# Optimization experiments

Measured on AMD Instinct MI355X. Metric: run time of the kernel, lower is better.

## Reference

```python
import jax, jax.numpy as jnp
import numpy as np

KS = 4          # kernel_size per pseudo-dim (open linear B-splines, degree 1)
GRID = 28       # level-0 grid side
BATCH = 256     # number of graphs
NUM_FIRST_FC = 49


def _grid(n, B):
    """Batched 8-neighborhood grid graph with 2D pseudo-coords in [0,1]."""
    rs, cs = np.meshgrid(np.arange(n), np.arange(n), indexing='ij')
    idx = rs * n + cs
    src_l, dst_l, ps_l = [], [], []
    for dr in (-1, 0, 1):
        for dc in (-1, 0, 1):
            if dr == 0 and dc == 0:
                continue
            r2, c2 = rs + dr, cs + dc
            ok = (r2 >= 0) & (r2 < n) & (c2 >= 0) & (c2 < n)
            src_l.append(idx[ok])
            dst_l.append((r2 * n + c2)[ok])
            m = int(ok.sum())
            ps_l.append(np.stack([np.full(m, (dr + 1) / 2.0),
                                  np.full(m, (dc + 1) / 2.0)], 1))
    src = np.concatenate(src_l)
    dst = np.concatenate(dst_l)
    pseudo = np.concatenate(ps_l).astype(np.float32)
    off = (np.arange(B) * n * n)[:, None]
    src_b = (src[None] + off).reshape(-1)
    dst_b = (dst[None] + off).reshape(-1)
    return (np.stack([src_b, dst_b]).astype(np.int32),
            np.tile(pseudo, (B, 1)))


def _cluster(n, B):
    """Factor-4 (2x2 block) graclus-style cluster assignment, batched."""
    rs, cs = np.meshgrid(np.arange(n), np.arange(n), indexing='ij')
    c = ((rs // 2) * (n // 2) + (cs // 2)).reshape(-1)
    off = (np.arange(B) * (n // 2) ** 2)[:, None]
    return (c[None] + off).reshape(-1).astype(np.int32)


def setup_inputs() -> dict:
    key = jax.random.key(0)
    ks = jax.random.split(key, 16)
    e0, p0 = _grid(GRID, BATCH)          # 28x28 level
    e1, p1 = _grid(GRID // 2, BATCH)     # 14x14 level
    c0 = _cluster(GRID, BATCH)           # 784 -> 196 per graph
    c1 = _cluster(GRID // 2, BATCH)      # 196 -> 49 per graph
    N0 = BATCH * GRID * GRID
    s = 0.1
    inp = {
        'x': jax.random.normal(ks[0], (N0, 1), jnp.float32),
        'edge_index0': jnp.asarray(e0), 'pseudo0': jnp.asarray(p0),
        'edge_index1': jnp.asarray(e1), 'pseudo1': jnp.asarray(p1),
        'cluster0': jnp.asarray(c0), 'cluster1': jnp.asarray(c1),
        'W1': s * jax.random.normal(ks[1], (16, 1, 32), jnp.float32),
        'root1': s * jax.random.normal(ks[2], (1, 32), jnp.float32),
        'b1': jnp.zeros((32,), jnp.float32),
        'W2': s * jax.random.normal(ks[3], (16, 32, 32), jnp.float32),
        'root2': s * jax.random.normal(ks[4], (32, 32), jnp.float32),
        'b2': jnp.zeros((32,), jnp.float32),
        'W3': s * jax.random.normal(ks[5], (16, 32, 64), jnp.float32),
        'root3': s * jax.random.normal(ks[6], (32, 64), jnp.float32),
        'b3': jnp.zeros((64,), jnp.float32),
        'W4': s * jax.random.normal(ks[7], (16, 64, 64), jnp.float32),
        'root4': s * jax.random.normal(ks[8], (64, 64), jnp.float32),
        'b4': jnp.zeros((64,), jnp.float32),
        'fc1_W': s * jax.random.normal(ks[9], (NUM_FIRST_FC * 64, 512), jnp.float32),
        'fc1_b': jnp.zeros((512,), jnp.float32),
        'fc2_W': s * jax.random.normal(ks[10], (512, 10), jnp.float32),
        'fc2_b': jnp.zeros((10,), jnp.float32),
    }
    return inp


def spline_conv(x, src, dst, pseudo, W, root, bias):
    """SplineGCN layer: degree-1 open B-spline weighting over 2D pseudo-coords,
    mean aggregation over incoming edges, plus root weight and bias."""
    n = x.shape[0]
    pos = pseudo * (KS - 1)                       # [E,2] in [0, KS-1]
    i0f = jnp.clip(jnp.floor(pos), 0, KS - 2)
    frac = pos - i0f                              # [E,2]
    i0 = i0f.astype(jnp.int32)
    XW = jnp.einsum('ni,kio->kno', x, W)          # [K, N, out]: per-kernel transform
    msg = jnp.zeros((src.shape[0], W.shape[2]), x.dtype)
    for a in (0, 1):
        wa = frac[:, 0] if a else 1.0 - frac[:, 0]
        for b in (0, 1):
            wb = frac[:, 1] if b else 1.0 - frac[:, 1]
            k = (i0[:, 0] + a) * KS + (i0[:, 1] + b)     # flat kernel index [E]
            msg = msg + (wa * wb)[:, None] * XW[k, src]  # gather per-edge
    agg = jax.ops.segment_sum(msg, dst, num_segments=n)
    deg = jax.ops.segment_sum(jnp.ones_like(dst, dtype=x.dtype), dst,
                              num_segments=n)
    return agg / jnp.maximum(deg, 1.0)[:, None] + x @ root + bias


def pool4(x, cluster):
    # GraclusMaxPool(2): two halving levels == factor-4 cluster max-pool
    return jax.ops.segment_max(x, cluster, num_segments=x.shape[0] // 4)


def reference(x, edge_index0, pseudo0, edge_index1, pseudo1, cluster0, cluster1,
              W1, root1, b1, W2, root2, b2, W3, root3, b3, W4, root4, b4,
              fc1_W, fc1_b, fc2_W, fc2_b):
    s0, d0 = edge_index0[0], edge_index0[1]
    s1, d1 = edge_index1[0], edge_index1[1]
    h = jax.nn.elu(spline_conv(x, s0, d0, pseudo0, W1, root1, b1))
    h = jax.nn.elu(spline_conv(h, s0, d0, pseudo0, W2, root2, b2))
    h = pool4(h, cluster0)
    h = jax.nn.elu(spline_conv(h, s1, d1, pseudo1, W3, root3, b3))
    h = jax.nn.elu(spline_conv(h, s1, d1, pseudo1, W4, root4, b4))
    h = pool4(h, cluster1)
    h = h.reshape(-1, NUM_FIRST_FC * 64)           # [B, 49*64]
    h = jax.nn.elu(h @ fc1_W + fc1_b)
    # dropout is identity in eval / deterministic reference
    logits = h @ fc2_W + fc2_b
    return jax.nn.log_softmax(logits, axis=-1)
```

## Files before the change

### kernel.cpp

```cpp
#include <hip/hip_runtime.h>

typedef unsigned short u16;
typedef short bf16x8 __attribute__((ext_vector_type(8)));
typedef float f32x4 __attribute__((ext_vector_type(4)));

__device__ __constant__ const int DRS[8] = {-1,-1,-1, 0, 0, 1, 1, 1};
__device__ __constant__ const int DCS[8] = {-1, 0, 1,-1, 1,-1, 0, 1};

__device__ inline float bf2f(u16 u) { return __uint_as_float(((unsigned)u) << 16); }
__device__ inline u16 f2bf(float f) {
  unsigned u = __float_as_uint(f);
  return (u16)((u + 0x7fffu + ((u >> 16) & 1u)) >> 16);
}
__device__ inline float eluf(float v) { return v > 0.f ? v : (__expf(v) - 1.f); }
__device__ inline unsigned pk2(float a, float b) {
  return (unsigned)f2bf(a) | ((unsigned)f2bf(b) << 16);
}

__device__ inline float weff_val(const float* __restrict__ W, int d, int off, int stride) {
  int dd = d >= 4 ? d + 1 : d;
  int dr = dd / 3 - 1, dc = dd - (dd / 3) * 3 - 1;
  int kr0, kr1, nr; float wr0, wr1;
  if (dr < 0)       { kr0 = 0; wr0 = 1.f; kr1 = 0; wr1 = 0.f; nr = 1; }
  else if (dr == 0) { kr0 = 1; wr0 = .5f; kr1 = 2; wr1 = .5f; nr = 2; }
  else              { kr0 = 3; wr0 = 1.f; kr1 = 0; wr1 = 0.f; nr = 1; }
  int kc0, kc1, nc; float wc0, wc1;
  if (dc < 0)       { kc0 = 0; wc0 = 1.f; kc1 = 0; wc1 = 0.f; nc = 1; }
  else if (dc == 0) { kc0 = 1; wc0 = .5f; kc1 = 2; wc1 = .5f; nc = 2; }
  else              { kc0 = 3; wc0 = 1.f; kc1 = 0; wc1 = 0.f; nc = 1; }
  float acc = wr0 * wc0 * W[(kr0 * 4 + kc0) * stride + off];
  if (nc == 2) acc += wr0 * wc1 * W[(kr0 * 4 + kc1) * stride + off];
  if (nr == 2) {
    acc += wr1 * wc0 * W[(kr1 * 4 + kc0) * stride + off];
    if (nc == 2) acc += wr1 * wc1 * W[(kr1 * 4 + kc1) * stride + off];
  }
  return acc;
}

__device__ inline int kperm32(int p) { return (p >> 1) + ((p & 1) << 4); }

__global__ __launch_bounds__(256) void pack_all(
    const float* __restrict__ W1,
    const float* __restrict__ W2, const float* __restrict__ rt2,
    const float* __restrict__ W3, const float* __restrict__ rt3,
    const float* __restrict__ W4, const float* __restrict__ rt4,
    const float* __restrict__ fcW,
    float* __restrict__ wf1, u16* __restrict__ wp2,
    u16* __restrict__ wp3, u16* __restrict__ wp4, u16* __restrict__ wfc) {
  __shared__ u16 T[32 * 514];
  int blk = blockIdx.x, t = threadIdx.x;
  if (blk < 98) {
    int q = blk;
#pragma unroll
    for (int i = 0; i < 16; ++i) {
      int idx = i * 1024 + t * 4;
      int k = idx >> 9, n = idx & 511;
      float4 v = *reinterpret_cast<const float4*>(fcW + (size_t)(q * 32 + k) * 512 + n);
      T[k * 514 + n]     = f2bf(v.x);
      T[k * 514 + n + 1] = f2bf(v.y);
      T[k * 514 + n + 2] = f2bf(v.z);
      T[k * 514 + n + 3] = f2bf(v.w);
    }
    __syncthreads();
#pragma unroll
    for (int w = 0; w < 8; ++w) {
      int g = w * 256 + t;
      int nt = g >> 6, l = g & 63;
      union { int4 q4; u16 s[8]; } R;
#pragma unroll
      for (int j = 0; j < 8; ++j)
        R.s[j] = T[((l >> 4) * 8 + j) * 514 + nt * 16 + (l & 15)];
      *reinterpret_cast<int4*>(wfc + ((size_t)(q * 32 + nt) * 64 + l) * 8) = R.q4;
    }
    return;
  }
  int idx = (blk - 98) * 256 + t;
  if (idx < 256) {
    int d = idx >> 5, o = idx & 31;
    wf1[idx] = weff_val(W1, d, o, 32);
    return;
  }
  if (idx < 9472) {
    int local = idx - 256;
    int j = local & 7, l = (local >> 3) & 63, chunk = local >> 9;
    int ct = chunk & 1, tap = chunk >> 1;
    int k = (l >> 4) * 8 + j, n = ct * 16 + (l & 15);
    float v = tap < 8 ? weff_val(W2, tap, k * 32 + n, 1024) : rt2[k * 32 + n];
    wp2[local] = f2bf(v);
    return;
  }
  if (idx < 27904) {
    int local = idx - 9472;
    int j = local & 7, l = (local >> 3) & 63, chunk = local >> 9;
    int ct = chunk & 3, tap = chunk >> 2;
    int k = kperm32((l >> 4) * 8 + j), n = ct * 16 + (l & 15);
    float v = tap < 8 ? weff_val(W3, tap, k * 64 + n, 2048) : rt3[k * 64 + n];
    wp3[local] = f2bf(v);
    return;
  }
  if (idx < 64768) {
    int local = idx - 27904;
    int j = local & 7, l = (local >> 3) & 63, chunk = local >> 9;
    int q = chunk & 1, tmp = chunk >> 1;
    int ct = tmp & 3, tap = tmp >> 2;
    int k = q * 32 + kperm32((l >> 4) * 8 + j), n = ct * 16 + (l & 15);
    float v = tap < 8 ? weff_val(W4, tap, k * 64 + n, 4096) : rt4[k * 64 + n];
    wp4[local] = f2bf(v);
  }
}

__global__ __launch_bounds__(1024, 2) void conv_mega(
    const float* __restrict__ x,
    const float* __restrict__ wf1, const float* __restrict__ rt1, const float* __restrict__ b1,
    const u16* __restrict__ wp2, const float* __restrict__ b2,
    const u16* __restrict__ wp3, const float* __restrict__ b3,
    const u16* __restrict__ wp4, const float* __restrict__ b4,
    u16* __restrict__ A6) {
  extern __shared__ char smem[];
  int4* H1 = (int4*)smem;
  int4* H3 = (int4*)smem;
  u16*  H5 = (u16*)(smem + 17408);
  int4* H4 = (int4*)(smem + 42496);
  unsigned* H4u = (unsigned*)(smem + 42496);
  float* XT = (float*)(smem + 61568);
  int4*     H2 = (int4*)(smem + 75520);
  unsigned* H2u = (unsigned*)(smem + 75520);

  int img = blockIdx.x, tid = threadIdx.x;
  int lane = tid & 63, wid = tid >> 6;
  int kcb = lane >> 4, n0 = lane & 15;
  int4 z4 = make_int4(0, 0, 0, 0);
  f32x4 zz = {0.f, 0.f, 0.f, 0.f};

  for (int i = tid; i < 3848; i += 1024) H1[i] = z4;
  if (tid < 960) {
    int r = tid >> 5, c = tid & 31;
    bool in = (r >= 1) && (r <= 28) && (c >= 1) && (c <= 28);
    XT[tid] = in ? x[(size_t)img * 784 + (r - 1) * 28 + (c - 1)] : 0.f;
  }
  __syncthreads();

  if (tid < 784) {
    int px = tid;
    int r = px / 28, c = px - 28 * (px / 28);
    float acc[32];
#pragma unroll
    for (int o = 0; o < 32; ++o) acc[o] = 0.f;
#pragma unroll
    for (int d = 0; d < 8; ++d) {
      float xv = XT[(r + 1 - DRS[d]) * 32 + (c + 1 - DCS[d])];
#pragma unroll
      for (int o = 0; o < 32; ++o) acc[o] = fmaf(xv, wf1[d * 32 + o], acc[o]);
    }
    float inv = 1.f / (float)((3 - (r == 0) - (r == 27)) * (3 - (c == 0) - (c == 27)) - 1);
    float xc = XT[(r + 1) * 32 + c + 1];
    unsigned pk[16];
#pragma unroll
    for (int h = 0; h < 16; ++h)
      pk[h] = pk2(eluf(acc[2 * h] * inv + xc * rt1[2 * h] + b1[2 * h]),
                  eluf(acc[2 * h + 1] * inv + xc * rt1[2 * h + 1] + b1[2 * h + 1]));
#pragma unroll
    for (int kc = 0; kc < 4; ++kc)
      H1[kc * 962 + (r + 1) * 32 + (c + 1)] =
          make_int4(pk[4 * kc], pk[4 * kc + 1], pk[4 * kc + 2], pk[4 * kc + 3]);
  }
  __syncthreads();

  {
    bf16x8 w2[9][2];
#pragma unroll
    for (int tap = 0; tap < 9; ++tap)
#pragma unroll
      for (int ct = 0; ct < 2; ++ct)
        w2[tap][ct] = *(const bf16x8*)(wp2 + (tap * 2 + ct) * 512 + lane * 8);
    for (int t = wid; t < 49; t += 16) {
      int pxm = t * 16 + n0;
      int r = pxm / 28, c = pxm - 28 * (pxm / 28);
      f32x4 an[2] = {zz, zz}, ar[2] = {zz, zz};
#pragma unroll
      for (int d = 0; d < 8; ++d) {
        bf16x8 a = *(const bf16x8*)&H1[kcb * 962 + (r + 1 - DRS[d]) * 32 + (c + 1 - DCS[d])];
        an[0] = __builtin_amdgcn_mfma_f32_16x16x32_bf16(a, w2[d][0], an[0], 0, 0, 0);
        an[1] = __builtin_amdgcn_mfma_f32_16x16x32_bf16(a, w2[d][1], an[1], 0, 0, 0);
      }
      {
        bf16x8 a = *(const bf16x8*)&H1[kcb * 962 + (r + 1) * 32 + (c + 1)];
        ar[0] = __builtin_amdgcn_mfma_f32_16x16x32_bf16(a, w2[8][0], ar[0], 0, 0, 0);
        ar[1] = __builtin_amdgcn_mfma_f32_16x16x32_bf16(a, w2[8][1], ar[1], 0, 0, 0);
      }
#pragma unroll
      for (int j = 0; j < 4; ++j) {
        int pm = t * 16 + (lane >> 4) * 4 + j;
        int rm = pm / 28, cm = pm - 28 * (pm / 28);
        float inv = 1.f / (float)((3 - (rm == 0) - (rm == 27)) * (3 - (cm == 0) - (cm == 27)) - 1);
        H2u[pm * 16 + n0] = pk2(eluf(an[0][j] * inv + ar[0][j] + b2[n0]),
                                eluf(an[1][j] * inv + ar[1][j] + b2[16 + n0]));
      }
    }
  }
  __syncthreads();

  for (int i = tid; i < 1032; i += 1024) {
    int kc = i & 3, rem = i >> 2;
    int4 v = z4;
    if (rem < 256) {
      int pr = rem >> 4, pc = rem & 15;
      if (pr >= 1 && pr <= 14 && pc >= 1 && pc <= 14) {
        int px0 = (2 * (pr - 1)) * 28 + 2 * (pc - 1);
        union { int4 q; u16 s[8]; } A, B, C, D, R;
        A.q = H2[px0 * 4 + kc]; B.q = H2[(px0 + 1) * 4 + kc];
        C.q = H2[(px0 + 28) * 4 + kc]; D.q = H2[(px0 + 29) * 4 + kc];
#pragma unroll
        for (int e = 0; e < 8; ++e)
          R.s[e] = f2bf(fmaxf(fmaxf(bf2f(A.s[e]), bf2f(B.s[e])),
                              fmaxf(bf2f(C.s[e]), bf2f(D.s[e]))));
        v = R.q;
      }
    }
    H3[kc * 258 + rem] = v;
  }
  for (int i = tid; i < 2064; i += 1024) H4[i] = z4;
  __syncthreads();

  {
    int ct0 = wid & 1, t0 = wid >> 1;
    bf16x8 w3[9][2];
#pragma unroll
    for (int tap = 0; tap < 9; ++tap)
#pragma unroll
      for (int cc = 0; cc < 2; ++cc)
        w3[tap][cc] = *(const bf16x8*)(wp3 + (tap * 4 + ct0 * 2 + cc) * 512 + lane * 8);
    for (int t = t0; t < 13; t += 8) {
      int pxm = t * 16 + n0; if (pxm > 195) pxm = 195;
      int r = pxm / 14, c = pxm - 14 * (pxm / 14);
      f32x4 an[2] = {zz, zz}, ar[2] = {zz, zz};
#pragma unroll
      for (int d = 0; d < 8; ++d) {
        bf16x8 a = *(const bf16x8*)&H3[kcb * 258 + (r + 1 - DRS[d]) * 16 + (c + 1 - DCS[d])];
        an[0] = __builtin_amdgcn_mfma_f32_16x16x32_bf16(a, w3[d][0], an[0], 0, 0, 0);
        an[1] = __builtin_amdgcn_mfma_f32_16x16x32_bf16(a, w3[d][1], an[1], 0, 0, 0);
      }
      {
        bf16x8 a = *(const bf16x8*)&H3[kcb * 258 + (r + 1) * 16 + (c + 1)];
        ar[0] = __builtin_amdgcn_mfma_f32_16x16x32_bf16(a, w3[8][0], ar[0], 0, 0, 0);
        ar[1] = __builtin_amdgcn_mfma_f32_16x16x32_bf16(a, w3[8][1], ar[1], 0, 0, 0);
      }
#pragma unroll
      for (int j = 0; j < 4; ++j) {
        int pm = t * 16 + (lane >> 4) * 4 + j;
        if (pm < 196) {
          int rm = pm / 14, cm = pm - 14 * (pm / 14);
          float inv = 1.f / (float)((3 - (rm == 0) - (rm == 13)) * (3 - (cm == 0) - (cm == 13)) - 1);
          unsigned v = pk2(eluf(an[0][j] * inv + ar[0][j] + b3[ct0 * 32 + n0]),
                           eluf(an[1][j] * inv + ar[1][j] + b3[ct0 * 32 + 16 + n0]));
          H4u[((ct0 * 4 + (n0 >> 2)) * 258 + (rm + 1) * 16 + (cm + 1)) * 4 + (n0 & 3)] = v;
        }
      }
    }
  }
  __syncthreads();

  {
    int ctg = wid & 3, t0 = wid >> 2;
    bf16x8 w4[9][2];
#pragma unroll
    for (int tap = 0; tap < 9; ++tap)
#pragma unroll
      for (int kq = 0; kq < 2; ++kq)
        w4[tap][kq] = *(const bf16x8*)(wp4 + ((tap * 4 + ctg) * 2 + kq) * 512 + lane * 8);
    for (int t = t0; t < 13; t += 4) {
      int pxm = t * 16 + n0; if (pxm > 195) pxm = 195;
      int r = pxm / 14, c = pxm - 14 * (pxm / 14);
      f32x4 an = zz, ar = zz;
#pragma unroll
      for (int d = 0; d < 8; ++d) {
        int rr = r + 1 - DRS[d], c2 = c + 1 - DCS[d];
#pragma unroll
        for (int kq = 0; kq < 2; ++kq) {
          bf16x8 a = *(const bf16x8*)&H4[(kq * 4 + kcb) * 258 + rr * 16 + c2];
          an = __builtin_amdgcn_mfma_f32_16x16x32_bf16(a, w4[d][kq], an, 0, 0, 0);
        }
      }
#pragma unroll
      for (int kq = 0; kq < 2; ++kq) {
        bf16x8 a = *(const bf16x8*)&H4[(kq * 4 + kcb) * 258 + (r + 1) * 16 + (c + 1)];
        ar = __builtin_amdgcn_mfma_f32_16x16x32_bf16(a, w4[8][kq], ar, 0, 0, 0);
      }
#pragma unroll
      for (int j = 0; j < 4; ++j) {
        int pm = t * 16 + (lane >> 4) * 4 + j;
        if (pm < 196) {
          int rm = pm / 14, cm = pm - 14 * (pm / 14);
          float inv = 1.f / (float)((3 - (rm == 0) - (rm == 13)) * (3 - (cm == 0) - (cm == 13)) - 1);
          int n = ctg * 16 + n0;
          H5[pm * 64 + n] = f2bf(eluf(an[j] * inv + ar[j] + b4[n]));
        }
      }
    }
  }
  __syncthreads();

  if (tid < 392) {
    int kc = tid & 7, q = tid >> 3;
    int r2 = q / 7, c2 = q - 7 * (q / 7);
    int px0 = (2 * r2) * 14 + 2 * c2;
    union { int4 q4; u16 s[8]; } A, B, C, D, R;
    A.q4 = *(const int4*)&H5[px0 * 64 + kc * 8];
    B.q4 = *(const int4*)&H5[(px0 + 1) * 64 + kc * 8];
    C.q4 = *(const int4*)&H5[(px0 + 14) * 64 + kc * 8];
    D.q4 = *(const int4*)&H5[(px0 + 15) * 64 + kc * 8];
#pragma unroll
    for (int e = 0; e < 8; ++e)
      R.s[e] = f2bf(fmaxf(fmaxf(bf2f(A.s[e]), bf2f(B.s[e])),
                          fmaxf(bf2f(C.s[e]), bf2f(D.s[e]))));
    *(int4*)(A6 + ((size_t)img * 49 + q) * 64 + kc * 8) = R.q4;
  }
}

__global__ __launch_bounds__(128) void fc1_mfma(
    const u16* __restrict__ A6, const u16* __restrict__ wfc,
    const float* __restrict__ fc1b, u16* __restrict__ h) {
  int blk = blockIdx.x;
  int mt = blk & 15, bn = blk >> 4;
  int lane = threadIdx.x & 63, w = threadIdx.x >> 6;
  int NT = bn * 2 + w;
  f32x4 acc0 = {0.f, 0.f, 0.f, 0.f}, acc1 = {0.f, 0.f, 0.f, 0.f};
  const u16* Ab = A6 + (size_t)(mt * 16 + (lane & 15)) * 3136 + (lane >> 4) * 8;
  const u16* Bb = wfc + (size_t)NT * 512 + (size_t)lane * 8;
#pragma unroll 7
  for (int qq = 0; qq < 98; qq += 2) {
    bf16x8 a0 = *(const bf16x8*)(Ab + qq * 32);
    bf16x8 b0 = *(const bf16x8*)(Bb + (size_t)qq * 16384);
    acc0 = __builtin_amdgcn_mfma_f32_16x16x32_bf16(a0, b0, acc0, 0, 0, 0);
    bf16x8 a1 = *(const bf16x8*)(Ab + qq * 32 + 32);
    bf16x8 b1 = *(const bf16x8*)(Bb + (size_t)qq * 16384 + 16384);
    acc1 = __builtin_amdgcn_mfma_f32_16x16x32_bf16(a1, b1, acc1, 0, 0, 0);
  }
#pragma unroll
  for (int j = 0; j < 4; ++j) {
    int row = mt * 16 + (lane >> 4) * 4 + j;
    int col = NT * 16 + (lane & 15);
    float v = acc0[j] + acc1[j] + fc1b[col];
    h[(size_t)row * 512 + col] = f2bf(eluf(v));
  }
}

__global__ __launch_bounds__(64) void fc2_kernel(
    const u16* __restrict__ h, const float* __restrict__ W,
    const float* __restrict__ bias, float* __restrict__ out) {
  int bb = blockIdx.x;
  int t = threadIdx.x;
  float acc[10];
#pragma unroll
  for (int o = 0; o < 10; ++o) acc[o] = 0.f;
  bf16x8 hv = *(const bf16x8*)(h + (size_t)bb * 512 + t * 8);
#pragma unroll
  for (int kk = 0; kk < 8; ++kk) {
    float xv = bf2f((u16)hv[kk]);
    int k = t * 8 + kk;
#pragma unroll
    for (int o = 0; o < 10; ++o) acc[o] = fmaf(xv, W[k * 10 + o], acc[o]);
  }
#pragma unroll
  for (int o = 0; o < 10; ++o) {
    float v = acc[o];
#pragma unroll
    for (int s = 32; s >= 1; s >>= 1) v += __shfl_xor(v, s);
    acc[o] = v + bias[o];
  }
  float m = acc[0];
#pragma unroll
  for (int o = 1; o < 10; ++o) m = fmaxf(m, acc[o]);
  float sum = 0.f;
#pragma unroll
  for (int o = 0; o < 10; ++o) sum += __expf(acc[o] - m);
  float lse = m + __logf(sum);
  if (t < 10) out[bb * 10 + t] = acc[t] - lse;
}

extern "C" void kernel_launch(void* const* d_in, const int* in_sizes, int n_in,
                              void* d_out, int out_size, void* d_ws, size_t ws_size,
                              hipStream_t stream) {
  const float* x    = (const float*)d_in[0];
  const float* W1   = (const float*)d_in[7];
  const float* r1   = (const float*)d_in[8];
  const float* b1   = (const float*)d_in[9];
  const float* W2   = (const float*)d_in[10];
  const float* r2   = (const float*)d_in[11];
  const float* b2   = (const float*)d_in[12];
  const float* W3   = (const float*)d_in[13];
  const float* r3   = (const float*)d_in[14];
  const float* b3   = (const float*)d_in[15];
  const float* W4   = (const float*)d_in[16];
  const float* r4   = (const float*)d_in[17];
  const float* b4   = (const float*)d_in[18];
  const float* fc1W = (const float*)d_in[19];
  const float* fc1b = (const float*)d_in[20];
  const float* fc2W = (const float*)d_in[21];
  const float* fc2b = (const float*)d_in[22];

  char* wsb = (char*)d_ws;
  float* wf1  = (float*)(wsb + 0);
  u16*   wp2  = (u16*)(wsb + 1024);
  u16*   wp3  = (u16*)(wsb + 19456);
  u16*   wp4  = (u16*)(wsb + 56320);
  u16*   wfc  = (u16*)(wsb + 130048);
  u16*   A6   = (u16*)(wsb + 3341312);
  u16*   hbuf = (u16*)(wsb + 4946944);

  pack_all<<<351, 256, 0, stream>>>(W1, W2, r2, W3, r3, W4, r4, fc1W,
                                    wf1, wp2, wp3, wp4, wfc);

  (void)hipFuncSetAttribute((const void*)conv_mega,
                            hipFuncAttributeMaxDynamicSharedMemorySize, 125696);
  conv_mega<<<256, 1024, 125696, stream>>>(x, wf1, r1, b1, wp2, b2, wp3, b3,
                                           wp4, b4, A6);

  fc1_mfma<<<256, 128, 0, stream>>>(A6, wfc, fc1b, hbuf);
  fc2_kernel<<<256, 64, 0, stream>>>(hbuf, fc2W, fc2b, (float*)d_out);
}
```

Measured before the change: 53.14 us.

## Move fc1 weight packing into conv kernel and restructure conv4 weight loads

The fc1 weight transpose and bf16 conversion moves out of the pack kernel into the first 98 blocks of the conv megakernel, with smem reused before the conv phases begin. The pack kernel shrinks to the small conv weights, so the conv kernel can start sooner. Conv4 now assigns two column tiles per wave and streams the B fragments from global memory instead of preloading 18 register fragments, cutting register pressure. The costs are extra preamble work in some conv blocks, which causes load imbalance, and repeated global or cache weight loads inside the MFMA loop.

```diff
diff --git a/kernel.cpp b/kernel.cpp
--- a/kernel.cpp
+++ b/kernel.cpp
@@ -39,42 +39,14 @@
 
 __device__ inline int kperm32(int p) { return (p >> 1) + ((p & 1) << 4); }
 
-__global__ __launch_bounds__(256) void pack_all(
+__global__ __launch_bounds__(256) void pack_small(
     const float* __restrict__ W1,
     const float* __restrict__ W2, const float* __restrict__ rt2,
     const float* __restrict__ W3, const float* __restrict__ rt3,
     const float* __restrict__ W4, const float* __restrict__ rt4,
-    const float* __restrict__ fcW,
     float* __restrict__ wf1, u16* __restrict__ wp2,
-    u16* __restrict__ wp3, u16* __restrict__ wp4, u16* __restrict__ wfc) {
-  __shared__ u16 T[32 * 514];
-  int blk = blockIdx.x, t = threadIdx.x;
-  if (blk < 98) {
-    int q = blk;
-#pragma unroll
-    for (int i = 0; i < 16; ++i) {
-      int idx = i * 1024 + t * 4;
-      int k = idx >> 9, n = idx & 511;
-      float4 v = *reinterpret_cast<const float4*>(fcW + (size_t)(q * 32 + k) * 512 + n);
-      T[k * 514 + n]     = f2bf(v.x);
-      T[k * 514 + n + 1] = f2bf(v.y);
-      T[k * 514 + n + 2] = f2bf(v.z);
-      T[k * 514 + n + 3] = f2bf(v.w);
-    }
-    __syncthreads();
-#pragma unroll
-    for (int w = 0; w < 8; ++w) {
-      int g = w * 256 + t;
-      int nt = g >> 6, l = g & 63;
-      union { int4 q4; u16 s[8]; } R;
-#pragma unroll
-      for (int j = 0; j < 8; ++j)
-        R.s[j] = T[((l >> 4) * 8 + j) * 514 + nt * 16 + (l & 15)];
-      *reinterpret_cast<int4*>(wfc + ((size_t)(q * 32 + nt) * 64 + l) * 8) = R.q4;
-    }
-    return;
-  }
-  int idx = (blk - 98) * 256 + t;
+    u16* __restrict__ wp3, u16* __restrict__ wp4) {
+  int idx = blockIdx.x * 256 + threadIdx.x;
   if (idx < 256) {
     int d = idx >> 5, o = idx & 31;
     wf1[idx] = weff_val(W1, d, o, 32);
@@ -115,6 +87,7 @@
     const u16* __restrict__ wp2, const float* __restrict__ b2,
     const u16* __restrict__ wp3, const float* __restrict__ b3,
     const u16* __restrict__ wp4, const float* __restrict__ b4,
+    const float* __restrict__ fcW, u16* __restrict__ wfc,
     u16* __restrict__ A6) {
   extern __shared__ char smem[];
   int4* H1 = (int4*)smem;
@@ -132,6 +105,33 @@
   int4 z4 = make_int4(0, 0, 0, 0);
   f32x4 zz = {0.f, 0.f, 0.f, 0.f};
 
+  if (img < 98) {
+    u16* T = (u16*)smem;
+    int q = img;
+#pragma unroll
+    for (int i = 0; i < 4; ++i) {
+      int idx = i * 4096 + tid * 4;
+      int k = idx >> 9, n = idx & 511;
+      float4 v = *reinterpret_cast<const float4*>(fcW + (size_t)(q * 32 + k) * 512 + n);
+      T[k * 514 + n]     = f2bf(v.x);
+      T[k * 514 + n + 1] = f2bf(v.y);
+      T[k * 514 + n + 2] = f2bf(v.z);
+      T[k * 514 + n + 3] = f2bf(v.w);
+    }
+    __syncthreads();
+#pragma unroll
+    for (int w = 0; w < 2; ++w) {
+      int g = w * 1024 + tid;
+      int nt = g >> 6, l = g & 63;
+      union { int4 q4; u16 s[8]; } R;
+#pragma unroll
+      for (int j = 0; j < 8; ++j)
+        R.s[j] = T[((l >> 4) * 8 + j) * 514 + nt * 16 + (l & 15)];
+      *reinterpret_cast<int4*>(wfc + ((size_t)(q * 32 + nt) * 64 + l) * 8) = R.q4;
+    }
+    __syncthreads();
+  }
+
   for (int i = tid; i < 3848; i += 1024) H1[i] = z4;
   if (tid < 960) {
     int r = tid >> 5, c = tid & 31;
@@ -261,30 +261,30 @@
   __syncthreads();
 
   {
-    int ctg = wid & 3, t0 = wid >> 2;
-    bf16x8 w4[9][2];
-#pragma unroll
-    for (int tap = 0; tap < 9; ++tap)
-#pragma unroll
-      for (int kq = 0; kq < 2; ++kq)
-        w4[tap][kq] = *(const bf16x8*)(wp4 + ((tap * 4 + ctg) * 2 + kq) * 512 + lane * 8);
-    for (int t = t0; t < 13; t += 4) {
+    int ct0 = wid & 1, t0 = wid >> 1;
+    for (int t = t0; t < 13; t += 8) {
       int pxm = t * 16 + n0; if (pxm > 195) pxm = 195;
       int r = pxm / 14, c = pxm - 14 * (pxm / 14);
-      f32x4 an = zz, ar = zz;
+      f32x4 an[2] = {zz, zz}, ar[2] = {zz, zz};
 #pragma unroll
       for (int d = 0; d < 8; ++d) {
         int rr = r + 1 - DRS[d], c2 = c + 1 - DCS[d];
 #pragma unroll
         for (int kq = 0; kq < 2; ++kq) {
           bf16x8 a = *(const bf16x8*)&H4[(kq * 4 + kcb) * 258 + rr * 16 + c2];
-          an = __builtin_amdgcn_mfma_f32_16x16x32_bf16(a, w4[d][kq], an, 0, 0, 0);
+          bf16x8 w0 = *(const bf16x8*)(wp4 + ((size_t)((d * 4 + ct0 * 2) * 2 + kq) * 64 + lane) * 8);
+          bf16x8 w1 = *(const bf16x8*)(wp4 + ((size_t)((d * 4 + ct0 * 2 + 1) * 2 + kq) * 64 + lane) * 8);
+          an[0] = __builtin_amdgcn_mfma_f32_16x16x32_bf16(a, w0, an[0], 0, 0, 0);
+          an[1] = __builtin_amdgcn_mfma_f32_16x16x32_bf16(a, w1, an[1], 0, 0, 0);
         }
       }
 #pragma unroll
       for (int kq = 0; kq < 2; ++kq) {
         bf16x8 a = *(const bf16x8*)&H4[(kq * 4 + kcb) * 258 + (r + 1) * 16 + (c + 1)];
-        ar = __builtin_amdgcn_mfma_f32_16x16x32_bf16(a, w4[8][kq], ar, 0, 0, 0);
+        bf16x8 w0 = *(const bf16x8*)(wp4 + ((size_t)((8 * 4 + ct0 * 2) * 2 + kq) * 64 + lane) * 8);
+        bf16x8 w1 = *(const bf16x8*)(wp4 + ((size_t)((8 * 4 + ct0 * 2 + 1) * 2 + kq) * 64 + lane) * 8);
+        ar[0] = __builtin_amdgcn_mfma_f32_16x16x32_bf16(a, w0, ar[0], 0, 0, 0);
+        ar[1] = __builtin_amdgcn_mfma_f32_16x16x32_bf16(a, w1, ar[1], 0, 0, 0);
       }
 #pragma unroll
       for (int j = 0; j < 4; ++j) {
@@ -292,8 +292,9 @@
         if (pm < 196) {
           int rm = pm / 14, cm = pm - 14 * (pm / 14);
           float inv = 1.f / (float)((3 - (rm == 0) - (rm == 13)) * (3 - (cm == 0) - (cm == 13)) - 1);
-          int n = ctg * 16 + n0;
-          H5[pm * 64 + n] = f2bf(eluf(an[j] * inv + ar[j] + b4[n]));
+          int na = ct0 * 32 + n0, nb = ct0 * 32 + 16 + n0;
+          H5[pm * 64 + na] = f2bf(eluf(an[0][j] * inv + ar[0][j] + b4[na]));
+          H5[pm * 64 + nb] = f2bf(eluf(an[1][j] * inv + ar[1][j] + b4[nb]));
         }
       }
     }
@@ -408,13 +409,13 @@
   u16*   A6   = (u16*)(wsb + 3341312);
   u16*   hbuf = (u16*)(wsb + 4946944);
 
-  pack_all<<<351, 256, 0, stream>>>(W1, W2, r2, W3, r3, W4, r4, fc1W,
-                                    wf1, wp2, wp3, wp4, wfc);
+  pack_small<<<253, 256, 0, stream>>>(W1, W2, r2, W3, r3, W4, r4,
+                                      wf1, wp2, wp3, wp4);
 
   (void)hipFuncSetAttribute((const void*)conv_mega,
                             hipFuncAttributeMaxDynamicSharedMemorySize, 125696);
   conv_mega<<<256, 1024, 125696, stream>>>(x, wf1, r1, b1, wp2, b2, wp3, b3,
-                                           wp4, b4, A6);
+                                           wp4, b4, fc1W, wfc, A6);
 
   fc1_mfma<<<256, 128, 0, stream>>>(A6, wfc, fc1b, hbuf);
   fc2_kernel<<<256, 64, 0, stream>>>(hbuf, fc2W, fc2b, (float*)d_out);
```

After: 72.90 us. 37.2% more time.
